# Kernel tuning notes

Hardware: AMD Instinct MI355X
Metric: run time of the kernel (lower is better)

## Reference

```python
import jax, jax.numpy as jnp
import numpy as np

B, J, D, K = 2048, 15, 9, 20
HID, NF = 256, 24


def _linear_params(key, fin, fout):
    kw, kb = jax.random.split(key)
    lim = 1.0 / np.sqrt(fin)
    W = jax.random.uniform(kw, (fin, fout), minval=-lim, maxval=lim, dtype=jnp.float32)
    b = jax.random.uniform(kb, (fout,), minval=-lim, maxval=lim, dtype=jnp.float32)
    return W, b


def setup_inputs() -> dict:
    key = jax.random.key(0)
    ks = jax.random.split(key, 9)
    inp = {"dct_input": jax.random.normal(ks[0], (B, J, D, K), dtype=jnp.float32)}
    inp["q_W1"], inp["q_b1"] = _linear_params(ks[1], K, HID)
    inp["q_W2"], inp["q_b2"] = _linear_params(ks[2], HID, HID)
    inp["k_W1"], inp["k_b1"] = _linear_params(ks[3], K, HID)
    inp["k_W2"], inp["k_b2"] = _linear_params(ks[4], HID, HID)
    inp["v_W1"], inp["v_b1"] = _linear_params(ks[5], K, HID)
    inp["v_W2"], inp["v_b2"] = _linear_params(ks[6], HID, HID)
    inp["p_W1"], inp["p_b1"] = _linear_params(ks[7], 2 * HID, HID)
    inp["p_W2"], inp["p_b2"] = _linear_params(ks[8], HID, NF)
    return inp


def _mlp(x, W1, b1, W2, b2):
    return jax.nn.relu(x @ W1 + b1) @ W2 + b2


def _idct_basis(n):
    # IDCT of DCT-II with norm='ortho' (scipy.fftpack.idct default type=2):
    # x[t] = sum_k c_k * X[k] * cos(pi*k*(2t+1)/(2n)), c_0=sqrt(1/n), c_k=sqrt(2/n)
    k = jnp.arange(n, dtype=jnp.float32)[:, None]
    t = jnp.arange(n, dtype=jnp.float32)[None, :]
    c = jnp.full((n, 1), np.sqrt(2.0 / n), dtype=jnp.float32).at[0, 0].set(np.sqrt(1.0 / n))
    return c * jnp.cos(np.pi * k * (2.0 * t + 1.0) / (2.0 * n))  # [k, t]


def reference(dct_input, q_W1, q_b1, q_W2, q_b2, k_W1, k_b1, k_W2, k_b2,
              v_W1, v_b1, v_W2, v_b2, p_W1, p_b1, p_W2, p_b2):
    b, j, d, kdim = dct_input.shape
    x = dct_input.reshape(b, j * d, kdim)          # tokens = J*D
    Q = _mlp(x, q_W1, q_b1, q_W2, q_b2)            # [B, T, H]
    Kt = _mlp(x, k_W1, k_b1, k_W2, k_b2)
    V = _mlp(x, v_W1, v_b1, v_W2, v_b2)
    scores = jnp.einsum('bth,bsh->bts', Q, Kt) / np.sqrt(Q.shape[-1])
    attn = jax.nn.softmax(scores, axis=-1)
    context = jnp.einsum('bts,bsh->bth', attn, V)
    feat = jnp.concatenate([Q, context], axis=-1)  # [B, T, 2H]
    out = _mlp(feat, p_W1, p_b1, p_W2, p_b2)       # [B, T, NF] (DCT coeffs)
    out = out.reshape(b, j, d, NF).transpose(0, 3, 1, 2)  # [B, NF, J, D]
    M = _idct_basis(NF)                            # [NF(k), NF(t)]
    time = jnp.einsum('bkjd,kt->btjd', out, M)     # inverse DCT along time axis
    pred = time.reshape(b, NF, j, 3, 3)
    return pred
```

## Files before the change

### kernel.cpp

```cpp
#include <hip/hip_runtime.h>

#define BDIM 512

typedef float f32x4 __attribute__((ext_vector_type(4)));
typedef short bf16x8 __attribute__((ext_vector_type(8)));

#define MFMA(a, b, c) __builtin_amdgcn_mfma_f32_16x16x32_bf16((a), (b), (c), 0, 0, 0)

constexpr int OQ1 = 0;
constexpr int OK1w = 8192;
constexpr int OV1 = 16384;
constexpr int OQ2 = 24576;
constexpr int OK2w = 90112;
constexpr int OV2 = 155648;
constexpr int OP1 = 221184;
constexpr int OP2 = 352256;
constexpr int WTOT = 360448;

constexpr int OFF_Q   = 0;
constexpr int OFF_XS  = 73728;
constexpr int OFF_SP  = 83968;
constexpr int OFF_HT2 = 127776;
constexpr int OFF_KVT = 144160;
constexpr int OFF_RWL = 160544;
constexpr int SMEM_BYTES = 161120;

constexpr int SPS = 152;

__device__ __forceinline__ unsigned short f2b(float f) {
  unsigned int u = __float_as_uint(f);
  return (unsigned short)((u + 0x7fffu + ((u >> 16) & 1u)) >> 16);
}
__device__ __forceinline__ float bfu(unsigned short u) {
  return __uint_as_float(((unsigned int)u) << 16);
}

__device__ __forceinline__ bf16x8 frag(const unsigned short* m, int rb, int stride,
                                       int kb, int lane) {
  return *(const bf16x8*)(m + (rb + (lane & 15)) * stride + kb + ((lane >> 4) << 3));
}
__device__ __forceinline__ bf16x8 frag256s(const unsigned short* m, int rb, int kb, int lane) {
  const int row = rb + (lane & 15);
  const int c = (kb + ((lane >> 4) << 3)) ^ ((row & 7) << 3);
  return *(const bf16x8*)(m + row * 256 + c);
}
__device__ __forceinline__ bf16x8 frag32s(const unsigned short* m, int rb, int lane) {
  const int row = rb + (lane & 15);
  const int c = ((lane >> 4) << 3) ^ (((row >> 1) & 3) << 3);
  return *(const bf16x8*)(m + row * 32 + c);
}
__device__ __forceinline__ int swz256(int r, int c) { return r * 256 + (c ^ ((r & 7) << 3)); }
__device__ __forceinline__ int swz32 (int r, int c) { return r * 32  + (c ^ (((r >> 1) & 3) << 3)); }

__global__ void prep_w(const float* __restrict__ qW1, const float* __restrict__ qW2,
                       const float* __restrict__ kW1, const float* __restrict__ kW2,
                       const float* __restrict__ vW1, const float* __restrict__ vW2,
                       const float* __restrict__ pW1, const float* __restrict__ pW2,
                       unsigned short* __restrict__ ws) {
  int i = blockIdx.x * 256 + threadIdx.x;
  if (i >= WTOT) return;
  float v = 0.f;
  if (i < OQ2) {
    int sel = i >> 13, r = i & 8191;
    int o = r >> 5, k = r & 31;
    const float* W = (sel == 0) ? qW1 : (sel == 1) ? kW1 : vW1;
    if (k < 20) v = W[k * 256 + o];
  } else if (i < OP1) {
    int r = i - OQ2;
    int sel = r >> 16, q = r & 65535;
    int o = q >> 8, k = q & 255;
    const float* W = (sel == 0) ? qW2 : (sel == 1) ? kW2 : vW2;
    v = W[k * 256 + o];
  } else if (i < OP2) {
    int r = i - OP1;
    int o = r >> 9, f = r & 511;
    v = pW1[f * 256 + o];
  } else {
    int r = i - OP2;
    int o = r >> 8, k = r & 255;
    if (o < 24) v = pW2[k * 24 + o];
  }
  ws[i] = f2b(v);
}

__global__ void g3_prep(const float* __restrict__ vW2, const float* __restrict__ pW1,
                        const float* __restrict__ pb1, const float* __restrict__ vb2,
                        unsigned short* __restrict__ ws) {
  __shared__ float col[256];
  __shared__ float red[256];
  const int o = blockIdx.x, c = threadIdx.x;
  col[c] = pW1[(256 + c) * 256 + o];
  __syncthreads();
  float acc = 0.f;
#pragma unroll 4
  for (int h = 0; h < 256; ++h) acc += vW2[c * 256 + h] * col[h];
  ws[OP1 + o * 512 + 256 + c] = f2b(acc);
  red[c] = vb2[c] * col[c];
  __syncthreads();
  for (int st = 128; st > 0; st >>= 1) {
    if (c < st) red[c] += red[c + st];
    __syncthreads();
  }
  if (c == 0) ((float*)(ws + OV2))[o] = pb1[o] + red[0];
}

__global__ __launch_bounds__(BDIM) __attribute__((amdgpu_waves_per_eu(2, 2)))
void motion_mfma(const float* __restrict__ x,
                 const float* __restrict__ qb1v, const float* __restrict__ qb2v,
                 const float* __restrict__ kb1v, const float* __restrict__ kb2v,
                 const float* __restrict__ vb1v, const float* __restrict__ vb2v,
                 const float* __restrict__ pb1v, const float* __restrict__ pb2v,
                 const unsigned short* __restrict__ ws,
                 float* __restrict__ out) {
  extern __shared__ char smem[];
  unsigned short* Qs  = (unsigned short*)(smem + OFF_Q);
  unsigned short* XS  = (unsigned short*)(smem + OFF_XS);
  unsigned short* SP  = (unsigned short*)(smem + OFF_SP);
  unsigned short* Hc  = (unsigned short*)(smem + OFF_SP);
  unsigned short* HT2 = (unsigned short*)(smem + OFF_HT2);
  unsigned short* KVT = (unsigned short*)(smem + OFF_KVT);
  unsigned short* VB0 = (unsigned short*)(smem + OFF_HT2);
  unsigned short* VB1 = (unsigned short*)(smem + OFF_KVT);
  float* RWL = (float*)(smem + OFF_RWL);
  float* Ob  = (float*)(smem + 0);
  float* MT  = (float*)(smem + 14400);

  const int tid = threadIdx.x, lane = tid & 63, w = tid >> 6;
  const int l15 = lane & 15, rs = ((lane >> 4) << 2);
  const int cb = w * 32;
  const int b = blockIdx.x;
  const f32x4 zf4 = {0.f, 0.f, 0.f, 0.f};
  const bf16x8 zb8 = {0, 0, 0, 0, 0, 0, 0, 0};

  const float* xb = x + (size_t)b * 2700;
  for (int i = tid; i < 160 * 32; i += BDIM) {
    int r = i >> 5, c = i & 31;
    float v = (r < 135 && c < 20) ? __builtin_nontemporal_load(xb + r * 20 + c) : 0.f;
    XS[swz32(r, c)] = f2b(v);
  }

  const bf16x8 kw0 = frag(ws + OK1w, cb, 32, 0, lane);
  const bf16x8 kw1 = frag(ws + OK1w, cb + 16, 32, 0, lane);
  const bf16x8 vw0 = frag(ws + OV1, cb, 32, 0, lane);
  const bf16x8 vw1 = frag(ws + OV1, cb + 16, 32, 0, lane);
  const float kbb0 = kb1v[cb + l15], kbb1 = kb1v[cb + 16 + l15];
  const float vbb0 = vb1v[cb + l15], vbb1 = vb1v[cb + 16 + l15];
  __syncthreads();

  auto L1 = [&](const bf16x8& u0, const bf16x8& u1, float bb0, float bb1, int s0) {
#pragma unroll
    for (int mm = 0; mm < 2; ++mm) {
      bf16x8 a = frag32s(XS, s0 + mm * 16, lane);
      f32x4 c0 = MFMA(a, u0, zf4), c1 = MFMA(a, u1, zf4);
#pragma unroll
      for (int r = 0; r < 4; ++r) {
        HT2[swz256(mm * 16 + rs + r, cb + l15)]      = f2b(fmaxf(c0[r] + bb0, 0.f));
        HT2[swz256(mm * 16 + rs + r, cb + 16 + l15)] = f2b(fmaxf(c1[r] + bb1, 0.f));
      }
    }
  };
  auto L1T = [&](int s0, unsigned short* buf) {
#pragma unroll
    for (int mm = 0; mm < 2; ++mm) {
      bf16x8 a = frag32s(XS, s0 + mm * 16, lane);
      f32x4 c0 = MFMA(a, vw0, zf4), c1 = MFMA(a, vw1, zf4);
#pragma unroll
      for (int r = 0; r < 4; ++r) {
        int tok = mm * 16 + rs + r;
        buf[swz32(cb + l15,      tok)] = f2b(fmaxf(c0[r] + vbb0, 0.f));
        buf[swz32(cb + 16 + l15, tok)] = f2b(fmaxf(c1[r] + vbb1, 0.f));
      }
    }
  };

  {
    bf16x8 w0 = frag(ws + OQ1, cb, 32, 0, lane);
    bf16x8 w1 = frag(ws + OQ1, cb + 16, 32, 0, lane);
    float bb0 = qb1v[cb + l15], bb1 = qb1v[cb + 16 + l15];
#pragma unroll
    for (int m = 0; m < 9; ++m) {
      bf16x8 a = frag32s(XS, m * 16, lane);
      f32x4 c0 = MFMA(a, w0, zf4);
      f32x4 c1 = MFMA(a, w1, zf4);
#pragma unroll
      for (int r = 0; r < 4; ++r) {
        Hc[swz256(m * 16 + rs + r, cb + l15)]      = f2b(fmaxf(c0[r] + bb0, 0.f));
        Hc[swz256(m * 16 + rs + r, cb + 16 + l15)] = f2b(fmaxf(c1[r] + bb1, 0.f));
      }
    }
  }
  __syncthreads();

  {
    f32x4 acc[9][2];
#pragma unroll
    for (int m = 0; m < 9; ++m) { acc[m][0] = zf4; acc[m][1] = zf4; }
#pragma unroll
    for (int ks = 0; ks < 8; ++ks) {
      bf16x8 g0 = frag(ws + OQ2, cb, 256, ks * 32, lane);
      bf16x8 g1 = frag(ws + OQ2, cb + 16, 256, ks * 32, lane);
#pragma unroll
      for (int m = 0; m < 9; ++m) {
        bf16x8 a = frag256s(Hc, m * 16, ks * 32, lane);
        acc[m][0] = MFMA(a, g0, acc[m][0]);
        acc[m][1] = MFMA(a, g1, acc[m][1]);
      }
    }
    float bb20 = qb2v[cb + l15], bb21 = qb2v[cb + 16 + l15];
#pragma unroll
    for (int m = 0; m < 9; ++m)
#pragma unroll
      for (int r = 0; r < 4; ++r) {
        Qs[swz256(m * 16 + rs + r, cb + l15)]      = f2b(acc[m][0][r] + bb20);
        Qs[swz256(m * 16 + rs + r, cb + 16 + l15)] = f2b(acc[m][1][r] + bb21);
      }
  }
  __syncthreads();

  L1(kw0, kw1, kbb0, kbb1, 0);
  __syncthreads();

  bf16x8 kg[8][2];
#pragma unroll
  for (int ks = 0; ks < 8; ++ks) {
    kg[ks][0] = frag(ws + OK2w, cb, 256, ks * 32, lane);
    kg[ks][1] = frag(ws + OK2w, cb + 16, 256, ks * 32, lane);
  }

  for (int ch = 0; ch < 5; ++ch) {
    const int s0 = ch * 32;
    {
      f32x4 a2[2][2] = {{zf4, zf4}, {zf4, zf4}};
#pragma unroll
      for (int ks = 0; ks < 8; ++ks) {
#pragma unroll
        for (int mm = 0; mm < 2; ++mm) {
          bf16x8 a = frag256s(HT2, mm * 16, ks * 32, lane);
          a2[mm][0] = MFMA(a, kg[ks][0], a2[mm][0]);
          a2[mm][1] = MFMA(a, kg[ks][1], a2[mm][1]);
        }
      }
      float bb0 = kb2v[cb + l15], bb1 = kb2v[cb + 16 + l15];
#pragma unroll
      for (int mm = 0; mm < 2; ++mm)
#pragma unroll
        for (int r = 0; r < 4; ++r) {
          KVT[swz256(mm * 16 + rs + r, cb + l15)]      = f2b(a2[mm][0][r] + bb0);
          KVT[swz256(mm * 16 + rs + r, cb + 16 + l15)] = f2b(a2[mm][1][r] + bb1);
        }
    }
    __syncthreads();
    if (ch < 4) L1(kw0, kw1, kbb0, kbb1, s0 + 32);
    else        L1T(0, VB0);
#pragma unroll
    for (int rep = 0; rep < 3; ++rep) {
      int j = w + rep * 8;
      if (j < 18) {
        int m = j >> 1, n = j & 1;
        int sb = s0 + n * 16;
        if (sb < 144) {
          f32x4 sa = zf4;
#pragma unroll
          for (int ks = 0; ks < 8; ++ks) {
            bf16x8 qa = frag256s(Qs, m * 16, ks * 32, lane);
            bf16x8 kf = frag256s(KVT, n * 16, ks * 32, lane);
            sa = MFMA(qa, kf, sa);
          }
#pragma unroll
          for (int r = 0; r < 4; ++r)
            SP[(m * 16 + rs + r) * SPS + sb + l15] = f2b(sa[r] * 0.0625f);
        }
      }
    }
    __syncthreads();
  }

#pragma unroll
  for (int pass = 0; pass < 2; ++pass) {
    int r = pass * 128 + (tid >> 2);
    if (r < 144) {
      int j = tid & 3;
      float mx = -1e30f;
      for (int s = j; s < 135; s += 4) mx = fmaxf(mx, bfu(SP[r * SPS + s]));
      mx = fmaxf(mx, __shfl_xor(mx, 1));
      mx = fmaxf(mx, __shfl_xor(mx, 2));
      float sum = 0.f;
      for (int s = j; s < 135; s += 4) {
        float p = __expf(bfu(SP[r * SPS + s]) - mx);
        SP[r * SPS + s] = f2b(p);
        sum += p;
      }
      sum += __shfl_xor(sum, 1);
      sum += __shfl_xor(sum, 2);
      if (j == 0) RWL[r] = sum;
      for (int s = 135 + j; s < 144; s += 4) SP[r * SPS + s] = 0;
    }
  }
  __syncthreads();

  f32x4 ctx[9][2];
#pragma unroll
  for (int m = 0; m < 9; ++m) { ctx[m][0] = zf4; ctx[m][1] = zf4; }
  for (int ch = 0; ch < 5; ++ch) {
    const int s0 = ch * 32;
    const unsigned short* rd = (ch & 1) ? VB1 : VB0;
    unsigned short* wr = (ch & 1) ? VB0 : VB1;
    if (ch < 4) L1T(s0 + 32, wr);
    {
      bf16x8 v0 = frag32s(rd, cb, lane);
      bf16x8 v1 = frag32s(rd, cb + 16, lane);
      const bool mask = (ch == 4) && (lane >= 32);
#pragma unroll
      for (int m = 0; m < 9; ++m) {
        bf16x8 pa = frag(SP, m * 16, SPS, s0, lane);
        if (mask) pa = zb8;
        ctx[m][0] = MFMA(pa, v0, ctx[m][0]);
        ctx[m][1] = MFMA(pa, v1, ctx[m][1]);
      }
    }
    __syncthreads();
  }

#pragma unroll
  for (int m = 0; m < 9; ++m)
#pragma unroll
    for (int r = 0; r < 4; ++r) {
      int t = m * 16 + rs + r;
      float inv = 1.0f / RWL[t];
      Hc[swz256(t, cb + l15)]      = f2b(ctx[m][0][r] * inv);
      Hc[swz256(t, cb + 16 + l15)] = f2b(ctx[m][1][r] * inv);
    }
  __syncthreads();

  {
    const float* pb1adj = (const float*)(ws + OV2);
    float pbias0 = pb1adj[cb + l15], pbias1 = pb1adj[cb + 16 + l15];
    f32x4 pacc[9][2];
#pragma unroll
    for (int m = 0; m < 9; ++m) {
      pacc[m][0] = (f32x4){pbias0, pbias0, pbias0, pbias0};
      pacc[m][1] = (f32x4){pbias1, pbias1, pbias1, pbias1};
    }
#pragma unroll
    for (int ks = 0; ks < 8; ++ks) {
      bf16x8 g0 = frag(ws + OP1, cb, 512, ks * 32, lane);
      bf16x8 g1 = frag(ws + OP1, cb + 16, 512, ks * 32, lane);
#pragma unroll
      for (int m = 0; m < 9; ++m) {
        bf16x8 a = frag256s(Qs, m * 16, ks * 32, lane);
        pacc[m][0] = MFMA(a, g0, pacc[m][0]);
        pacc[m][1] = MFMA(a, g1, pacc[m][1]);
      }
    }
#pragma unroll
    for (int ks = 0; ks < 8; ++ks) {
      bf16x8 g0 = frag(ws + OP1, cb, 512, 256 + ks * 32, lane);
      bf16x8 g1 = frag(ws + OP1, cb + 16, 512, 256 + ks * 32, lane);
#pragma unroll
      for (int m = 0; m < 9; ++m) {
        bf16x8 a = frag256s(Hc, m * 16, ks * 32, lane);
        pacc[m][0] = MFMA(a, g0, pacc[m][0]);
        pacc[m][1] = MFMA(a, g1, pacc[m][1]);
      }
    }
    __syncthreads();
#pragma unroll
    for (int m = 0; m < 9; ++m)
#pragma unroll
      for (int r = 0; r < 4; ++r) {
        Hc[swz256(m * 16 + rs + r, cb + l15)]      = f2b(fmaxf(pacc[m][0][r], 0.f));
        Hc[swz256(m * 16 + rs + r, cb + 16 + l15)] = f2b(fmaxf(pacc[m][1][r], 0.f));
      }
  }
  for (int i = tid; i < 576; i += BDIM) {
    int kk = i / 24, t = i - kk * 24;
    float c = (kk == 0) ? 0.20412414523193150f : 0.28867513459481287f;
    MT[i] = c * cosf(0.065449846949787352f * (float)(kk * (2 * t + 1)));
  }
  __syncthreads();

#pragma unroll
  for (int rep = 0; rep < 3; ++rep) {
    int j = w + rep * 8;
    if (j < 18) {
      int m = j >> 1, n = j & 1;
      f32x4 oa = zf4;
#pragma unroll
      for (int ks = 0; ks < 8; ++ks) {
        bf16x8 a = frag256s(Hc, m * 16, ks * 32, lane);
        bf16x8 g = frag(ws + OP2, n * 16, 256, ks * 32, lane);
        oa = MFMA(a, g, oa);
      }
      int c = n * 16 + l15;
      if (c < 24) {
        float bb = pb2v[c];
#pragma unroll
        for (int r = 0; r < 4; ++r)
          Ob[(m * 16 + rs + r) * 25 + c] = oa[r] + bb;
      }
    }
  }
  __syncthreads();

  for (int i = tid; i < 3240; i += BDIM) {
    int tt = i / 135, tok = i - tt * 135;
    float a = 0.f;
#pragma unroll
    for (int k = 0; k < 24; ++k)
      a = fmaf(Ob[tok * 25 + k], MT[k * 24 + tt], a);
    __builtin_nontemporal_store(a, out + (size_t)b * 3240 + i);
  }
}

extern "C" void kernel_launch(void* const* d_in, const int* in_sizes, int n_in,
                              void* d_out, int out_size, void* d_ws, size_t ws_size,
                              hipStream_t stream) {
  (void)in_sizes; (void)n_in; (void)out_size;
  if (ws_size < (size_t)WTOT * 2) return;

  const float* x   = (const float*)d_in[0];
  const float* qW1 = (const float*)d_in[1];
  const float* qb1 = (const float*)d_in[2];
  const float* qW2 = (const float*)d_in[3];
  const float* qb2 = (const float*)d_in[4];
  const float* kW1 = (const float*)d_in[5];
  const float* kb1 = (const float*)d_in[6];
  const float* kW2 = (const float*)d_in[7];
  const float* kb2 = (const float*)d_in[8];
  const float* vW1 = (const float*)d_in[9];
  const float* vb1 = (const float*)d_in[10];
  const float* vW2 = (const float*)d_in[11];
  const float* vb2 = (const float*)d_in[12];
  const float* pW1 = (const float*)d_in[13];
  const float* pb1 = (const float*)d_in[14];
  const float* pW2 = (const float*)d_in[15];
  const float* pb2 = (const float*)d_in[16];
  float* out = (float*)d_out;
  unsigned short* ws = (unsigned short*)d_ws;

  prep_w<<<dim3((WTOT + 255) / 256), dim3(256), 0, stream>>>(
      qW1, qW2, kW1, kW2, vW1, vW2, pW1, pW2, ws);
  g3_prep<<<dim3(256), dim3(256), 0, stream>>>(vW2, pW1, pb1, vb2, ws);

  (void)hipFuncSetAttribute((const void*)motion_mfma,
                            hipFuncAttributeMaxDynamicSharedMemorySize, SMEM_BYTES);
  motion_mfma<<<dim3(2048), dim3(BDIM), SMEM_BYTES, stream>>>(
      x, qb1, qb2, kb1, kb2, vb1, vb2, pb1, pb2, ws, out);
}
```

Measured before the change: 539.5 us.

## Fold Q and K second-layer weights algebraically to skip the K projection GEMM

Precomputes W2q·W2kᵀ and folds it into the query path, so attention scores are taken directly against the K hidden activations. The K second-layer GEMM and its per-chunk barrier go away; the K bias is dropped because it only adds a per-row constant that softmax cancels. qW2 is also folded into the first projection weight, and the raw Q hidden layer is recomputed into the Q buffer for the output MLP. In exchange the kernel does an extra first-layer recompute, adds two small prep kernels, and rounds the fused weight products to bf16, which changes numerics slightly.

Result: slower. 686.1 us (+27.2%).

```diff
diff --git a/kernel.cpp b/kernel.cpp
--- a/kernel.cpp
+++ b/kernel.cpp
@@ -104,12 +104,52 @@
   if (c == 0) ((float*)(ws + OV2))[o] = pb1[o] + red[0];
 }
 
+__global__ void g2_prep(const float* __restrict__ qW2, const float* __restrict__ kW2,
+                        const float* __restrict__ qb2, unsigned short* __restrict__ ws) {
+  __shared__ float krow[256];
+  __shared__ float red[256];
+  const int h = blockIdx.x, g = threadIdx.x;
+  krow[g] = kW2[h * 256 + g];
+  __syncthreads();
+  float acc = 0.f;
+#pragma unroll 4
+  for (int o = 0; o < 256; ++o) acc += qW2[g * 256 + o] * krow[o];
+  ws[OQ2 + h * 256 + g] = f2b(acc);
+  red[g] = qb2[g] * krow[g];
+  __syncthreads();
+  for (int st = 128; st > 0; st >>= 1) {
+    if (g < st) red[g] += red[g + st];
+    __syncthreads();
+  }
+  if (g == 0) ((float*)(ws + OV2))[256 + h] = red[0];
+}
+
+__global__ void g4_prep(const float* __restrict__ qW2, const float* __restrict__ pW1,
+                        const float* __restrict__ qb2, unsigned short* __restrict__ ws) {
+  __shared__ float col[256];
+  __shared__ float red[256];
+  const int n = blockIdx.x, k = threadIdx.x;
+  col[k] = pW1[k * 256 + n];
+  __syncthreads();
+  float acc = 0.f;
+#pragma unroll 4
+  for (int o = 0; o < 256; ++o) acc += qW2[k * 256 + o] * col[o];
+  ws[OP1 + n * 512 + k] = f2b(acc);
+  red[k] = qb2[k] * col[k];
+  __syncthreads();
+  for (int st = 128; st > 0; st >>= 1) {
+    if (k < st) red[k] += red[k + st];
+    __syncthreads();
+  }
+  if (k == 0) ((float*)(ws + OV2))[n] += red[0];
+}
+
 __global__ __launch_bounds__(BDIM) __attribute__((amdgpu_waves_per_eu(2, 2)))
 void motion_mfma(const float* __restrict__ x,
-                 const float* __restrict__ qb1v, const float* __restrict__ qb2v,
-                 const float* __restrict__ kb1v, const float* __restrict__ kb2v,
-                 const float* __restrict__ vb1v, const float* __restrict__ vb2v,
-                 const float* __restrict__ pb1v, const float* __restrict__ pb2v,
+                 const float* __restrict__ qb1v,
+                 const float* __restrict__ kb1v,
+                 const float* __restrict__ vb1v,
+                 const float* __restrict__ pb2v,
                  const unsigned short* __restrict__ ws,
                  float* __restrict__ out) {
   extern __shared__ char smem[];
@@ -119,8 +159,6 @@
   unsigned short* Hc  = (unsigned short*)(smem + OFF_SP);
   unsigned short* HT2 = (unsigned short*)(smem + OFF_HT2);
   unsigned short* KVT = (unsigned short*)(smem + OFF_KVT);
-  unsigned short* VB0 = (unsigned short*)(smem + OFF_HT2);
-  unsigned short* VB1 = (unsigned short*)(smem + OFF_KVT);
   float* RWL = (float*)(smem + OFF_RWL);
   float* Ob  = (float*)(smem + 0);
   float* MT  = (float*)(smem + 14400);
@@ -139,23 +177,27 @@
     XS[swz32(r, c)] = f2b(v);
   }
 
+  const bf16x8 qw0 = frag(ws + OQ1, cb, 32, 0, lane);
+  const bf16x8 qw1 = frag(ws + OQ1, cb + 16, 32, 0, lane);
   const bf16x8 kw0 = frag(ws + OK1w, cb, 32, 0, lane);
   const bf16x8 kw1 = frag(ws + OK1w, cb + 16, 32, 0, lane);
   const bf16x8 vw0 = frag(ws + OV1, cb, 32, 0, lane);
   const bf16x8 vw1 = frag(ws + OV1, cb + 16, 32, 0, lane);
+  const float qbb0 = qb1v[cb + l15], qbb1 = qb1v[cb + 16 + l15];
   const float kbb0 = kb1v[cb + l15], kbb1 = kb1v[cb + 16 + l15];
   const float vbb0 = vb1v[cb + l15], vbb1 = vb1v[cb + 16 + l15];
   __syncthreads();
 
-  auto L1 = [&](const bf16x8& u0, const bf16x8& u1, float bb0, float bb1, int s0) {
+  auto L1 = [&](const bf16x8& u0, const bf16x8& u1, float bb0, float bb1,
+                int s0, unsigned short* buf) {
 #pragma unroll
     for (int mm = 0; mm < 2; ++mm) {
       bf16x8 a = frag32s(XS, s0 + mm * 16, lane);
       f32x4 c0 = MFMA(a, u0, zf4), c1 = MFMA(a, u1, zf4);
 #pragma unroll
       for (int r = 0; r < 4; ++r) {
-        HT2[swz256(mm * 16 + rs + r, cb + l15)]      = f2b(fmaxf(c0[r] + bb0, 0.f));
-        HT2[swz256(mm * 16 + rs + r, cb + 16 + l15)] = f2b(fmaxf(c1[r] + bb1, 0.f));
+        buf[swz256(mm * 16 + rs + r, cb + l15)]      = f2b(fmaxf(c0[r] + bb0, 0.f));
+        buf[swz256(mm * 16 + rs + r, cb + 16 + l15)] = f2b(fmaxf(c1[r] + bb1, 0.f));
       }
     }
   };
@@ -172,26 +214,25 @@
       }
     }
   };
-
-  {
-    bf16x8 w0 = frag(ws + OQ1, cb, 32, 0, lane);
-    bf16x8 w1 = frag(ws + OQ1, cb + 16, 32, 0, lane);
-    float bb0 = qb1v[cb + l15], bb1 = qb1v[cb + 16 + l15];
+  auto QL1full = [&](unsigned short* dst) {
 #pragma unroll
     for (int m = 0; m < 9; ++m) {
       bf16x8 a = frag32s(XS, m * 16, lane);
-      f32x4 c0 = MFMA(a, w0, zf4);
-      f32x4 c1 = MFMA(a, w1, zf4);
+      f32x4 c0 = MFMA(a, qw0, zf4);
+      f32x4 c1 = MFMA(a, qw1, zf4);
 #pragma unroll
       for (int r = 0; r < 4; ++r) {
-        Hc[swz256(m * 16 + rs + r, cb + l15)]      = f2b(fmaxf(c0[r] + bb0, 0.f));
-        Hc[swz256(m * 16 + rs + r, cb + 16 + l15)] = f2b(fmaxf(c1[r] + bb1, 0.f));
-      }
-    }
-  }
+        dst[swz256(m * 16 + rs + r, cb + l15)]      = f2b(fmaxf(c0[r] + qbb0, 0.f));
+        dst[swz256(m * 16 + rs + r, cb + 16 + l15)] = f2b(fmaxf(c1[r] + qbb1, 0.f));
+      }
+    }
+  };
+
+  QL1full(Hc);
   __syncthreads();
 
   {
+    const float* qb2t = ((const float*)(ws + OV2)) + 256;
     f32x4 acc[9][2];
 #pragma unroll
     for (int m = 0; m < 9; ++m) { acc[m][0] = zf4; acc[m][1] = zf4; }
@@ -206,7 +247,7 @@
         acc[m][1] = MFMA(a, g1, acc[m][1]);
       }
     }
-    float bb20 = qb2v[cb + l15], bb21 = qb2v[cb + 16 + l15];
+    float bb20 = qb2t[cb + l15], bb21 = qb2t[cb + 16 + l15];
 #pragma unroll
     for (int m = 0; m < 9; ++m)
 #pragma unroll
@@ -217,41 +258,15 @@
   }
   __syncthreads();
 
-  L1(kw0, kw1, kbb0, kbb1, 0);
-  __syncthreads();
-
-  bf16x8 kg[8][2];
-#pragma unroll
-  for (int ks = 0; ks < 8; ++ks) {
-    kg[ks][0] = frag(ws + OK2w, cb, 256, ks * 32, lane);
-    kg[ks][1] = frag(ws + OK2w, cb + 16, 256, ks * 32, lane);
-  }
-
+  L1(kw0, kw1, kbb0, kbb1, 0, HT2);
+  __syncthreads();
+
+  unsigned short* kb_[2] = {HT2, KVT};
   for (int ch = 0; ch < 5; ++ch) {
     const int s0 = ch * 32;
-    {
-      f32x4 a2[2][2] = {{zf4, zf4}, {zf4, zf4}};
-#pragma unroll
-      for (int ks = 0; ks < 8; ++ks) {
-#pragma unroll
-        for (int mm = 0; mm < 2; ++mm) {
-          bf16x8 a = frag256s(HT2, mm * 16, ks * 32, lane);
-          a2[mm][0] = MFMA(a, kg[ks][0], a2[mm][0]);
-          a2[mm][1] = MFMA(a, kg[ks][1], a2[mm][1]);
-        }
-      }
-      float bb0 = kb2v[cb + l15], bb1 = kb2v[cb + 16 + l15];
-#pragma unroll
-      for (int mm = 0; mm < 2; ++mm)
-#pragma unroll
-        for (int r = 0; r < 4; ++r) {
-          KVT[swz256(mm * 16 + rs + r, cb + l15)]      = f2b(a2[mm][0][r] + bb0);
-          KVT[swz256(mm * 16 + rs + r, cb + 16 + l15)] = f2b(a2[mm][1][r] + bb1);
-        }
-    }
-    __syncthreads();
-    if (ch < 4) L1(kw0, kw1, kbb0, kbb1, s0 + 32);
-    else        L1T(0, VB0);
+    const unsigned short* cur = kb_[ch & 1];
+    if (ch < 4) L1(kw0, kw1, kbb0, kbb1, s0 + 32, kb_[(ch + 1) & 1]);
+    else        L1T(0, KVT);
 #pragma unroll
     for (int rep = 0; rep < 3; ++rep) {
       int j = w + rep * 8;
@@ -263,7 +278,7 @@
 #pragma unroll
           for (int ks = 0; ks < 8; ++ks) {
             bf16x8 qa = frag256s(Qs, m * 16, ks * 32, lane);
-            bf16x8 kf = frag256s(KVT, n * 16, ks * 32, lane);
+            bf16x8 kf = frag256s(cur, n * 16, ks * 32, lane);
             sa = MFMA(qa, kf, sa);
           }
 #pragma unroll
@@ -303,8 +318,8 @@
   for (int m = 0; m < 9; ++m) { ctx[m][0] = zf4; ctx[m][1] = zf4; }
   for (int ch = 0; ch < 5; ++ch) {
     const int s0 = ch * 32;
-    const unsigned short* rd = (ch & 1) ? VB1 : VB0;
-    unsigned short* wr = (ch & 1) ? VB0 : VB1;
+    const unsigned short* rd = (ch & 1) ? HT2 : KVT;
+    unsigned short* wr = (ch & 1) ? KVT : HT2;
     if (ch < 4) L1T(s0 + 32, wr);
     {
       bf16x8 v0 = frag32s(rd, cb, lane);
@@ -330,6 +345,7 @@
       Hc[swz256(t, cb + l15)]      = f2b(ctx[m][0][r] * inv);
       Hc[swz256(t, cb + 16 + l15)] = f2b(ctx[m][1][r] * inv);
     }
+  QL1full(Qs);
   __syncthreads();
 
   {
@@ -426,7 +442,6 @@
   const float* kW1 = (const float*)d_in[5];
   const float* kb1 = (const float*)d_in[6];
   const float* kW2 = (const float*)d_in[7];
-  const float* kb2 = (const float*)d_in[8];
   const float* vW1 = (const float*)d_in[9];
   const float* vb1 = (const float*)d_in[10];
   const float* vW2 = (const float*)d_in[11];
@@ -441,9 +456,11 @@
   prep_w<<<dim3((WTOT + 255) / 256), dim3(256), 0, stream>>>(
       qW1, qW2, kW1, kW2, vW1, vW2, pW1, pW2, ws);
   g3_prep<<<dim3(256), dim3(256), 0, stream>>>(vW2, pW1, pb1, vb2, ws);
+  g2_prep<<<dim3(256), dim3(256), 0, stream>>>(qW2, kW2, qb2, ws);
+  g4_prep<<<dim3(256), dim3(256), 0, stream>>>(qW2, pW1, qb2, ws);
 
   (void)hipFuncSetAttribute((const void*)motion_mfma,
                             hipFuncAttributeMaxDynamicSharedMemorySize, SMEM_BYTES);
   motion_mfma<<<dim3(2048), dim3(BDIM), SMEM_BYTES, stream>>>(
-      x, qb1, qb2, kb1, kb2, vb1, vb2, pb1, pb2, ws, out);
-}
+      x, qb1, kb1, vb1, pb2, ws, out);
+}
```
